# Optimization experiments

Measured on AMD Instinct MI355X. Metric: run time of the kernel, lower is better.

The kernel has to match this reference:

```python
import jax, jax.numpy as jnp
import numpy as np
from jax import lax

NPOINT, RADIUS, NSAMPLE = 1024, 0.2, 32
BN_EPS = 1e-5


def square_distance(src, dst):
    # src [B,N,C], dst [B,M,C] -> [B,N,M] squared euclidean distances
    d = -2.0 * jnp.einsum('bnc,bmc->bnm', src, dst)
    d = d + jnp.sum(src ** 2, -1)[:, :, None]
    d = d + jnp.sum(dst ** 2, -1)[:, None, :]
    return d


def index_points(points, idx):
    # points [B,N,C], idx [B,...] int -> [B,...,C]
    B = points.shape[0]
    bidx = jnp.arange(B).reshape((B,) + (1,) * (idx.ndim - 1))
    return points[bidx, idx]


def farthest_point_sample(xyz, npoint):
    # Deterministic variant: first centroid is point 0 (torch code uses randint).
    B, N, C = xyz.shape
    def step(carry, _):
        distance, farthest = carry
        centroid = jnp.take_along_axis(xyz, farthest[:, None, None], axis=1)  # [B,1,C]
        dist = jnp.sum((xyz - centroid) ** 2, -1)  # [B,N]
        distance = jnp.minimum(distance, dist)
        nxt = jnp.argmax(distance, -1).astype(jnp.int32)
        return (distance, nxt), farthest
    init = (jnp.full((B, N), 1e10, xyz.dtype), jnp.zeros((B,), jnp.int32))
    _, cents = lax.scan(step, init, None, length=npoint)  # [npoint, B]
    return cents.T  # [B, npoint]


def query_ball_point(radius, nsample, xyz, new_xyz):
    B, N, _ = xyz.shape
    sqr = square_distance(new_xyz, xyz)  # [B,M,N]
    gidx = jnp.where(sqr > radius ** 2, N, jnp.arange(N, dtype=jnp.int32))
    gidx = jnp.sort(gidx, axis=-1)[:, :, :nsample]  # [B,M,nsample]
    first = gidx[:, :, 0:1]
    return jnp.where(gidx == N, first, gidx)


def setup_inputs() -> dict:
    key = jax.random.key(0)
    ks = jax.random.split(key, 5)
    B, N, D = 16, 4096, 64
    xyz = jax.random.uniform(ks[0], (B, N, 3), dtype=jnp.float32)
    points = jax.random.normal(ks[1], (B, N, D), dtype=jnp.float32)
    W0 = jax.random.normal(ks[2], (64, 67), dtype=jnp.float32) * 0.05
    W1 = jax.random.normal(ks[3], (64, 64), dtype=jnp.float32) * 0.05
    W2 = jax.random.normal(ks[4], (128, 64), dtype=jnp.float32) * 0.05
    return {
        'xyz': xyz, 'points': points,
        'W0': W0, 'g0': jnp.ones((64,), jnp.float32), 'b0': jnp.zeros((64,), jnp.float32),
        'W1': W1, 'g1': jnp.ones((64,), jnp.float32), 'b1': jnp.zeros((64,), jnp.float32),
        'W2': W2, 'g2': jnp.ones((128,), jnp.float32), 'b2': jnp.zeros((128,), jnp.float32),
    }


def reference(xyz, points, W0, g0, b0, W1, g1, b1, W2, g2, b2):
    B, N, C = xyz.shape
    fps_idx = farthest_point_sample(xyz, NPOINT)             # [B,M]
    new_xyz = index_points(xyz, fps_idx)                     # [B,M,3]
    idx = query_ball_point(RADIUS, NSAMPLE, xyz, new_xyz)    # [B,M,S]
    grouped_xyz = index_points(xyz, idx) - new_xyz[:, :, None, :]   # [B,M,S,3]
    x = jnp.concatenate([index_points(points, idx), grouped_xyz], -1)  # [B,M,S,67]
    # shared 1x1 conv + BatchNorm (training-mode batch stats, biased var) + ReLU
    for W, g, b in ((W0, g0, b0), (W1, g1, b1), (W2, g2, b2)):
        x = jnp.einsum('bmsc,oc->bmso', x, W)
        mean = jnp.mean(x, axis=(0, 1, 2))
        var = jnp.var(x, axis=(0, 1, 2))
        x = jax.nn.relu((x - mean) * jax.lax.rsqrt(var + BN_EPS) * g + b)
    new_points = jnp.max(x, axis=2)  # max over nsample -> [B,M,128]
    return (new_xyz, new_points)
```

## Files before the change

kernel.cpp:

```cpp
#include <hip/hip_runtime.h>
#include <hip/hip_bf16.h>
#include <cstdint>
#include <cstddef>

namespace {
constexpr int B_ = 16;
constexpr int N_ = 4096;
constexpr int D_ = 64;
constexpr int M_ = 1024;
constexpr int S_ = 32;
constexpr int NROWS_ = B_ * M_ * S_;
constexpr int TPB_ = 256;
constexpr int NBLKM_ = NROWS_ / TPB_;
constexpr int NBLK2_ = NROWS_ / (2 * TPB_);
constexpr float RR_ = 0.04f;

constexpr size_t OFF_SQN  = 0;
constexpr size_t OFF_FPS  = 262144;
constexpr size_t OFF_BALL = 327680;
constexpr size_t OFF_W0T  = 2424832;
constexpr size_t OFF_W1T  = OFF_W0T + 67 * 64 * 4;
constexpr size_t OFF_W2T  = OFF_W1T + 64 * 64 * 4;
constexpr size_t OFF_PART = OFF_W2T + 64 * 128 * 4;
constexpr size_t OFF_BNP  = OFF_PART + (size_t)NBLKM_ * 256 * 4;
constexpr size_t OFF_E    = (OFF_BNP + 3072 + 255) & ~(size_t)255;
constexpr size_t E_SZ     = (size_t)B_ * N_ * 64 * 4;
constexpr size_t OFF_D    = OFF_E + E_SZ;
constexpr size_t D_SZ     = (size_t)B_ * M_ * 64 * 4;
constexpr size_t OFF_H1   = OFF_D + D_SZ;
constexpr size_t H1F_SZ   = (size_t)NROWS_ * 64 * 4;
constexpr size_t H1H_SZ   = (size_t)NROWS_ * 64 * 2;
constexpr size_t NEED_A   = OFF_H1 + H1F_SZ;
constexpr size_t NEED_B   = OFF_H1 + H1H_SZ;
}

__device__ __forceinline__ float mul_nr(float a, float b) {
    float p = a * b;
    asm("" : "+v"(p));
    return p;
}
__device__ __forceinline__ float mul_nf(float a, float b) {
    float p = a * b;
    asm volatile("" : "+v"(p));
    return p;
}

template <int CTRL>
__device__ __forceinline__ float dpp_movf(float x) {
    return __int_as_float(
        __builtin_amdgcn_update_dpp(0, __float_as_int(x), CTRL, 0xF, 0xF, true));
}
__device__ __forceinline__ float xor_exch(float x, int k) {
    if (k == 0) return dpp_movf<0xB1>(x);
    if (k == 1) return dpp_movf<0x4E>(x);
    return __shfl_xor(x, 1 << k);
}

__device__ __forceinline__ float fold_sum_wave(float* cur, int lane) {
#pragma unroll
    for (int k = 0; k < 6; k++) {
        const bool hi = (lane >> k) & 1;
#pragma unroll
        for (int m = 0; m < (32 >> k); m++) {
            const float a = cur[2 * m], b = cur[2 * m + 1];
            const float keep = hi ? b : a;
            const float give = hi ? a : b;
            const float got = xor_exch(give, k);
            cur[m] = keep + got;
        }
    }
    return cur[0];
}
__device__ __forceinline__ float fold_sum32(float* cur, int lane) {
#pragma unroll
    for (int k = 0; k < 5; k++) {
        const bool hi = (lane >> k) & 1;
#pragma unroll
        for (int m = 0; m < (16 >> k); m++) {
            const float a = cur[2 * m], b = cur[2 * m + 1];
            const float keep = hi ? b : a;
            const float give = hi ? a : b;
            const float got = xor_exch(give, k);
            cur[m] = keep + got;
        }
    }
    return cur[0];
}
__device__ __forceinline__ float fold_max32(float* cur, int lane) {
#pragma unroll
    for (int k = 0; k < 5; k++) {
        const bool hi = (lane >> k) & 1;
#pragma unroll
        for (int m = 0; m < (16 >> k); m++) {
            const float a = cur[2 * m], b = cur[2 * m + 1];
            const float keep = hi ? b : a;
            const float give = hi ? a : b;
            const float got = xor_exch(give, k);
            cur[m] = fmaxf(keep, got);
        }
    }
    return cur[0];
}
__device__ __forceinline__ float fold_min32(float* cur, int lane) {
#pragma unroll
    for (int k = 0; k < 5; k++) {
        const bool hi = (lane >> k) & 1;
#pragma unroll
        for (int m = 0; m < (16 >> k); m++) {
            const float a = cur[2 * m], b = cur[2 * m + 1];
            const float keep = hi ? b : a;
            const float give = hi ? a : b;
            const float got = xor_exch(give, k);
            cur[m] = fminf(keep, got);
        }
    }
    return cur[0];
}
__device__ __forceinline__ void fold_max_half(float* cur, int lane, float& r0, float& r1) {
#pragma unroll
    for (int k = 0; k < 5; k++) {
        const bool hi = (lane >> k) & 1;
#pragma unroll
        for (int m = 0; m < (32 >> k); m++) {
            const float a = cur[2 * m], b = cur[2 * m + 1];
            const float keep = hi ? b : a;
            const float give = hi ? a : b;
            const float got = xor_exch(give, k);
            cur[m] = fmaxf(keep, got);
        }
    }
    r0 = cur[0]; r1 = cur[1];
}

__device__ __forceinline__ unsigned short f2bf(float f) {
    __hip_bfloat16 h = __float2bfloat16(f);
    return *reinterpret_cast<unsigned short*>(&h);
}
__device__ __forceinline__ float bf2f(unsigned short u) {
    __hip_bfloat16 h = *reinterpret_cast<__hip_bfloat16*>(&u);
    return __bfloat162float(h);
}

__global__ __launch_bounds__(256) void k_sqnorm(const float* __restrict__ xyz,
                                                float* __restrict__ sqn) {
    int i = blockIdx.x * 256 + threadIdx.x;
    if (i >= B_ * N_) return;
    float x = xyz[3 * i], y = xyz[3 * i + 1], z = xyz[3 * i + 2];
    sqn[i] = (mul_nf(x, x) + mul_nf(y, y)) + mul_nf(z, z);
}

__global__ __launch_bounds__(512) void k_fps(const float* __restrict__ xyz,
                                             int* __restrict__ fps_idx) {
    const int b = blockIdx.x, t = threadIdx.x;
    const int lane = t & 63, w = t >> 6;
    const float* xb = xyz + (size_t)b * N_ * 3;
    __shared__ float pts[N_ * 3];
    __shared__ unsigned long long slots[2][8];
    for (int i = t; i < N_ * 3; i += 512) pts[i] = xb[i];
    __syncthreads();

    const int n0 = t * 8;
    float px[8], py[8], pz[8], dist[8];
#pragma unroll
    for (int k = 0; k < 8; k++) {
        px[k] = pts[3 * (n0 + k)];
        py[k] = pts[3 * (n0 + k) + 1];
        pz[k] = pts[3 * (n0 + k) + 2];
        dist[k] = 1e10f;
    }

    int far = 0;
    for (int i = 0; i < M_; i++) {
        if (t == 0) fps_idx[b * M_ + i] = far;
        const float c0 = pts[3 * far], c1 = pts[3 * far + 1], c2 = pts[3 * far + 2];
        float bestv = -1.0f; int bestn = n0;
#pragma unroll
        for (int k = 0; k < 8; k++) {
            const float d0 = px[k] - c0, d1 = py[k] - c1, d2 = pz[k] - c2;
            const float dd = (mul_nr(d0, d0) + mul_nr(d1, d1)) + mul_nr(d2, d2);
            const float dm = fminf(dist[k], dd);
            dist[k] = dm;
            if (dm > bestv) { bestv = dm; bestn = n0 + k; }
        }
        float m = bestv;
        m = fmaxf(m, dpp_movf<0x111>(m));
        m = fmaxf(m, dpp_movf<0x112>(m));
        m = fmaxf(m, dpp_movf<0x114>(m));
        m = fmaxf(m, dpp_movf<0x118>(m));
        m = fmaxf(m, dpp_movf<0x142>(m));
        m = fmaxf(m, dpp_movf<0x143>(m));
        const float wmax = __int_as_float(
            __builtin_amdgcn_readlane(__float_as_int(m), 63));
        const unsigned long long mk = __ballot(bestv == wmax);
        const int src = __ffsll((long long)mk) - 1;
        const int wn = __builtin_amdgcn_readlane(bestn, src);
        if (lane == 0)
            slots[i & 1][w] =
                ((unsigned long long)__float_as_uint(wmax) << 32) | (unsigned)(~wn);
        __syncthreads();
        const unsigned long long* sl = slots[i & 1];
        const unsigned long long s0 = sl[0], s1 = sl[1], s2 = sl[2], s3 = sl[3];
        const unsigned long long s4 = sl[4], s5 = sl[5], s6 = sl[6], s7 = sl[7];
        const unsigned long long a0 = s0 > s1 ? s0 : s1;
        const unsigned long long a1 = s2 > s3 ? s2 : s3;
        const unsigned long long a2 = s4 > s5 ? s4 : s5;
        const unsigned long long a3 = s6 > s7 ? s6 : s7;
        const unsigned long long b0 = a0 > a1 ? a0 : a1;
        const unsigned long long b1 = a2 > a3 ? a2 : a3;
        const unsigned long long bb = b0 > b1 ? b0 : b1;
        far = (int)(~(unsigned)bb);
    }
}

__global__ __launch_bounds__(256) void k_newxyz(const float* __restrict__ xyz,
                                                const int* __restrict__ fps_idx,
                                                float* __restrict__ newxyz) {
    int i = blockIdx.x * 256 + threadIdx.x;
    if (i >= B_ * M_) return;
    int b = i >> 10;
    int f = fps_idx[i];
    const float* p = xyz + ((size_t)b * N_ + f) * 3;
    newxyz[3 * i] = p[0]; newxyz[3 * i + 1] = p[1]; newxyz[3 * i + 2] = p[2];
}

__global__ __launch_bounds__(256) void k_ball(const float* __restrict__ xyz,
                                              const float* __restrict__ sqn,
                                              const int* __restrict__ fps_idx,
                                              const float* __restrict__ newxyz,
                                              int* __restrict__ ball) {
    const int w = threadIdx.x >> 6, lane = threadIdx.x & 63;
    const int q = blockIdx.x * 4 + w;
    const int b = q >> 10;
    __shared__ int buf[4][32];
    const float* xb = xyz + (size_t)b * N_ * 3;
    const float* sb = sqn + (size_t)b * N_;
    const float q0 = newxyz[3 * q], q1 = newxyz[3 * q + 1], q2 = newxyz[3 * q + 2];
    const float sq = sb[fps_idx[q]];

    int cnt = 0;
    for (int base = 0; base < N_ && cnt < 32; base += 64) {
        const int n = base + lane;
        const float p0 = xb[3 * n], p1 = xb[3 * n + 1], p2 = xb[3 * n + 2];
        float dot = fmaf(q2, p2, fmaf(q1, p1, q0 * p0));
        float tt = -2.0f * dot;
        tt = tt + sq;
        tt = tt + sb[n];
        const bool pred = !(tt > RR_);
        const unsigned long long mask = __ballot(pred);
        const int pos = cnt + __popcll(mask & ((1ull << lane) - 1ull));
        if (pred && pos < 32) buf[w][pos] = n;
        cnt += (int)__popcll(mask);
    }
    __syncthreads();
    if (lane < 32) {
        int e = buf[w][(lane < cnt) ? lane : 0];
        ball[(size_t)q * 32 + lane] = e;
    }
}

__global__ __launch_bounds__(256) void k_wtrans(const float* __restrict__ W0,
                                                const float* __restrict__ W1,
                                                const float* __restrict__ W2,
                                                float* __restrict__ W0T,
                                                float* __restrict__ W1T,
                                                float* __restrict__ W2T) {
    int t = blockIdx.x * 256 + threadIdx.x;
    if (t < 64 * 67) { int o = t / 67, c = t % 67; W0T[c * 64 + o] = W0[t]; }
    if (t < 64 * 64) { int o = t / 64, c = t % 64; W1T[c * 64 + o] = W1[t]; }
    if (t < 128 * 64) { int o = t / 64, c = t % 64; W2T[c * 128 + o] = W2[t]; }
}

__device__ __forceinline__ void stage_w(float* dst, const float* __restrict__ src,
                                        int n, int t) {
    for (int i = t; i < n; i += TPB_) dst[i] = src[i];
}

template <int NCH>
__device__ __forceinline__ void bn_relu(float* x, const float* __restrict__ bnp, int base) {
#pragma unroll
    for (int o = 0; o < NCH; o++)
        x[o] = fmaxf(0.f, fmaf(x[o], bnp[base + o], bnp[base + 128 + o]));
}

__device__ __forceinline__ void load_h0(float* x, const float* __restrict__ E,
                                        const float* __restrict__ Dq,
                                        const int* __restrict__ ball, int r) {
    const int b = r >> 15, q = r >> 5;
    const int g = ball[r];
    const float4* e = (const float4*)(E + ((size_t)(b * N_) + g) * 64);
    const float4* d = (const float4*)(Dq + (size_t)q * 64);
#pragma unroll
    for (int j = 0; j < 16; j++) {
        const float4 ev = e[j]; const float4 dv = d[j];
        x[4 * j + 0] = ev.x - dv.x; x[4 * j + 1] = ev.y - dv.y;
        x[4 * j + 2] = ev.z - dv.z; x[4 * j + 3] = ev.w - dv.w;
    }
}

__device__ __forceinline__ void h1_load_f32(float* x, const float* buf, int r) {
    const float4* src = (const float4*)(buf + (size_t)r * 64);
#pragma unroll
    for (int j = 0; j < 16; j++) {
        const float4 v = src[j];
        x[4 * j] = v.x; x[4 * j + 1] = v.y; x[4 * j + 2] = v.z; x[4 * j + 3] = v.w;
    }
}
__device__ __forceinline__ void h1_load_bf(float* x, const unsigned short* buf, int r) {
    const ushort4* src = (const ushort4*)(buf + (size_t)r * 64);
#pragma unroll
    for (int j = 0; j < 16; j++) {
        const ushort4 v = src[j];
        x[4 * j] = bf2f(v.x); x[4 * j + 1] = bf2f(v.y);
        x[4 * j + 2] = bf2f(v.z); x[4 * j + 3] = bf2f(v.w);
    }
}

__global__ __launch_bounds__(TPB_) void k_e(
    const float* __restrict__ points, const float* __restrict__ xyz,
    const float* __restrict__ W0T, float* __restrict__ E) {
    __shared__ float w0[67 * 64];
    const int t = threadIdx.x;
    stage_w(w0, W0T, 67 * 64, t);
    __syncthreads();
    const int n = blockIdx.x * TPB_ + t;
    const float* prow = points + (size_t)n * 64;
    float h[64];
#pragma unroll
    for (int o = 0; o < 64; o++) h[o] = 0.f;
#pragma unroll
    for (int c = 0; c < 64; c += 4) {
        const float4 xv = *reinterpret_cast<const float4*>(prow + c);
        const float xs[4] = {xv.x, xv.y, xv.z, xv.w};
#pragma unroll
        for (int j = 0; j < 4; j++) {
            const float xc = xs[j];
            const float* wr = w0 + (c + j) * 64;
#pragma unroll
            for (int o = 0; o < 64; o++) h[o] = fmaf(xc, wr[o], h[o]);
        }
    }
    const float x0 = xyz[(size_t)n * 3], x1 = xyz[(size_t)n * 3 + 1], x2 = xyz[(size_t)n * 3 + 2];
#pragma unroll
    for (int o = 0; o < 64; o++) h[o] = fmaf(x0, w0[64 * 64 + o], h[o]);
#pragma unroll
    for (int o = 0; o < 64; o++) h[o] = fmaf(x1, w0[65 * 64 + o], h[o]);
#pragma unroll
    for (int o = 0; o < 64; o++) h[o] = fmaf(x2, w0[66 * 64 + o], h[o]);
    float4* dst = (float4*)(E + (size_t)n * 64);
#pragma unroll
    for (int j = 0; j < 16; j++)
        dst[j] = make_float4(h[4 * j], h[4 * j + 1], h[4 * j + 2], h[4 * j + 3]);
}

__global__ __launch_bounds__(256) void k_d(
    const float* __restrict__ newxyz, const float* __restrict__ W0T,
    float* __restrict__ Dq) {
    const int q = blockIdx.x * 256 + threadIdx.x;
    const float n0 = newxyz[3 * q], n1 = newxyz[3 * q + 1], n2 = newxyz[3 * q + 2];
    const float* wa = W0T + 64 * 64;
    const float* wb = W0T + 65 * 64;
    const float* wc = W0T + 66 * 64;
    float* dst = Dq + (size_t)q * 64;
#pragma unroll
    for (int o = 0; o < 64; o++)
        dst[o] = fmaf(n2, wc[o], fmaf(n1, wb[o], n0 * wa[o]));
}

__global__ __launch_bounds__(TPB_, 2) void k_s0(
    const float* __restrict__ E, const float* __restrict__ Dq,
    const int* __restrict__ ball, float* __restrict__ partials) {
    const int t = threadIdx.x, lane = t & 63, w = t >> 6;
    const int r0 = blockIdx.x * 512 + t, r1 = r0 + 256;
    __shared__ float ssum[4][64], ssq[4][64];
    float x0[64], x1[64];
    load_h0(x0, E, Dq, ball, r0);
    load_h0(x1, E, Dq, ball, r1);
#pragma unroll
    for (int i = 0; i < 64; i++) {
        const float sv_ = x0[i] + x1[i];
        x1[i] = x0[i] * x0[i] + x1[i] * x1[i];
        x0[i] = sv_;
    }
    const float sv = fold_sum_wave(x0, lane);
    const float qv = fold_sum_wave(x1, lane);
    ssum[w][lane] = sv; ssq[w][lane] = qv;
    __syncthreads();
    if (t < 64) {
        float* dst = partials + (size_t)blockIdx.x * 256;
        dst[t] = ssum[0][t] + ssum[1][t] + ssum[2][t] + ssum[3][t];
        dst[128 + t] = ssq[0][t] + ssq[1][t] + ssq[2][t] + ssq[3][t];
    }
}

template <int HST>
__global__ __launch_bounds__(TPB_, 2) void k_s1(
    const float* __restrict__ E, const float* __restrict__ Dq,
    const int* __restrict__ ball, const float* __restrict__ W1T,
    const float* __restrict__ bnp, float* __restrict__ partials,
    float* __restrict__ h1f, unsigned short* __restrict__ h1h) {
    __shared__ float w1[64 * 64];
    __shared__ float ssum[4][64], ssq[4][64];
    const int t = threadIdx.x, lane = t & 63, w = t >> 6;
    stage_w(w1, W1T, 64 * 64, t);
    const int r0 = blockIdx.x * 512 + t, r1 = r0 + 256;
    float x0[64], x1[64];
    load_h0(x0, E, Dq, ball, r0);
    bn_relu<64>(x0, bnp, 0);
    load_h0(x1, E, Dq, ball, r1);
    bn_relu<64>(x1, bnp, 0);
    __syncthreads();

#pragma unroll
    for (int tile = 0; tile < 2; tile++) {
        float a0[32], a1[32];
#pragma unroll
        for (int o = 0; o < 32; o++) { a0[o] = 0.f; a1[o] = 0.f; }
#pragma unroll
        for (int c = 0; c < 64; c++) {
            const float* wr = w1 + c * 64 + tile * 32;
            const float xc0 = x0[c], xc1 = x1[c];
#pragma unroll
            for (int o = 0; o < 32; o++) {
                a0[o] = fmaf(xc0, wr[o], a0[o]);
                a1[o] = fmaf(xc1, wr[o], a1[o]);
            }
        }
        if constexpr (HST == 1) {
            float4* d0 = (float4*)(h1f + (size_t)r0 * 64 + tile * 32);
            float4* d1 = (float4*)(h1f + (size_t)r1 * 64 + tile * 32);
#pragma unroll
            for (int j = 0; j < 8; j++) {
                d0[j] = make_float4(a0[4 * j], a0[4 * j + 1], a0[4 * j + 2], a0[4 * j + 3]);
                d1[j] = make_float4(a1[4 * j], a1[4 * j + 1], a1[4 * j + 2], a1[4 * j + 3]);
            }
        } else {
            ushort4* d0 = (ushort4*)(h1h + (size_t)r0 * 64 + tile * 32);
            ushort4* d1 = (ushort4*)(h1h + (size_t)r1 * 64 + tile * 32);
#pragma unroll
            for (int j = 0; j < 8; j++) {
                ushort4 v0, v1;
                v0.x = f2bf(a0[4 * j]); v0.y = f2bf(a0[4 * j + 1]);
                v0.z = f2bf(a0[4 * j + 2]); v0.w = f2bf(a0[4 * j + 3]);
                v1.x = f2bf(a1[4 * j]); v1.y = f2bf(a1[4 * j + 1]);
                v1.z = f2bf(a1[4 * j + 2]); v1.w = f2bf(a1[4 * j + 3]);
                d0[j] = v0; d1[j] = v1;
            }
        }
#pragma unroll
        for (int o = 0; o < 32; o++) {
            const float sv_ = a0[o] + a1[o];
            a1[o] = a0[o] * a0[o] + a1[o] * a1[o];
            a0[o] = sv_;
        }
        float sv = fold_sum32(a0, lane); sv += __shfl_xor(sv, 32);
        float qv = fold_sum32(a1, lane); qv += __shfl_xor(qv, 32);
        if (lane < 32) { ssum[w][tile * 32 + lane] = sv; ssq[w][tile * 32 + lane] = qv; }
    }
    __syncthreads();
    if (t < 64) {
        float* dst = partials + (size_t)blockIdx.x * 256;
        dst[t] = ssum[0][t] + ssum[1][t] + ssum[2][t] + ssum[3][t];
        dst[128 + t] = ssq[0][t] + ssq[1][t] + ssq[2][t] + ssq[3][t];
    }
}

template <int HLD>
__global__ __launch_bounds__(TPB_, 2) void k_s2(
    const float* __restrict__ h1f, const unsigned short* __restrict__ h1h,
    const float* __restrict__ W2T, const float* __restrict__ bnp,
    float* __restrict__ partials, float* __restrict__ maxb,
    float* __restrict__ minb) {
    __shared__ float w2[64 * 128];
    __shared__ float ssum[4][128], ssq[4][128];
    const int t = threadIdx.x, lane = t & 63, w = t >> 6;
    stage_w(w2, W2T, 64 * 128, t);
    const int r0 = blockIdx.x * 512 + t, r1 = r0 + 256;
    float x0[64], x1[64];
    if constexpr (HLD == 1) { h1_load_f32(x0, h1f, r0); h1_load_f32(x1, h1f, r1); }
    else { h1_load_bf(x0, h1h, r0); h1_load_bf(x1, h1h, r1); }
    bn_relu<64>(x0, bnp, 256);
    bn_relu<64>(x1, bnp, 256);
    __syncthreads();

    const int q0 = blockIdx.x * 16 + w * 2 + (lane >> 5);
#pragma unroll
    for (int tile = 0; tile < 4; tile++) {
        float a0[32], a1[32];
#pragma unroll
        for (int o = 0; o < 32; o++) { a0[o] = 0.f; a1[o] = 0.f; }
#pragma unroll
        for (int c = 0; c < 64; c++) {
            const float* wr = w2 + c * 128 + tile * 32;
            const float xc0 = x0[c], xc1 = x1[c];
#pragma unroll
            for (int o = 0; o < 32; o++) {
                a0[o] = fmaf(xc0, wr[o], a0[o]);
                a1[o] = fmaf(xc1, wr[o], a1[o]);
            }
        }
        {
            float c0[32];
#pragma unroll
            for (int o = 0; o < 32; o++) c0[o] = a0[o];
            const float mx = fold_max32(c0, lane);
#pragma unroll
            for (int o = 0; o < 32; o++) c0[o] = a0[o];
            const float mn = fold_min32(c0, lane);
            maxb[(size_t)q0 * 128 + tile * 32 + (lane & 31)] = mx;
            minb[(size_t)q0 * 128 + tile * 32 + (lane & 31)] = mn;
#pragma unroll
            for (int o = 0; o < 32; o++) c0[o] = a1[o];
            const float mx1 = fold_max32(c0, lane);
#pragma unroll
            for (int o = 0; o < 32; o++) c0[o] = a1[o];
            const float mn1 = fold_min32(c0, lane);
            maxb[(size_t)(q0 + 8) * 128 + tile * 32 + (lane & 31)] = mx1;
            minb[(size_t)(q0 + 8) * 128 + tile * 32 + (lane & 31)] = mn1;
        }
#pragma unroll
        for (int o = 0; o < 32; o++) {
            const float sv_ = a0[o] + a1[o];
            a1[o] = a0[o] * a0[o] + a1[o] * a1[o];
            a0[o] = sv_;
        }
        float sv = fold_sum32(a0, lane); sv += __shfl_xor(sv, 32);
        float qv = fold_sum32(a1, lane); qv += __shfl_xor(qv, 32);
        if (lane < 32) { ssum[w][tile * 32 + lane] = sv; ssq[w][tile * 32 + lane] = qv; }
    }
    __syncthreads();
    if (t < 128) {
        float* dst = partials + (size_t)blockIdx.x * 256;
        dst[t] = ssum[0][t] + ssum[1][t] + ssum[2][t] + ssum[3][t];
        dst[128 + t] = ssq[0][t] + ssq[1][t] + ssq[2][t] + ssq[3][t];
    }
}

__global__ __launch_bounds__(256) void k_s3m(
    const float* __restrict__ maxb, const float* __restrict__ minb,
    const float* __restrict__ bnp, float* __restrict__ out_np) {
    const int i = blockIdx.x * 256 + threadIdx.x;
    const int ch = i & 127;
    const float sc = bnp[512 + ch], sh = bnp[512 + 128 + ch];
    const float h = (sc >= 0.f) ? maxb[i] : minb[i];
    out_np[i] = fmaxf(0.f, fmaf(h, sc, sh));
}

__device__ __forceinline__ void g0_row(
    const float* __restrict__ points, const float* __restrict__ xyz,
    const float* __restrict__ newxyz, const int* __restrict__ ball,
    const float* w0, int r, float* h0) {
    const int b = r >> 15;
    const int q = r >> 5;
    const int g = ball[r];
    const float* prow = points + ((size_t)(b * N_) + g) * D_;
    const float xg0 = xyz[((size_t)b * N_ + g) * 3 + 0] - newxyz[(size_t)q * 3 + 0];
    const float xg1 = xyz[((size_t)b * N_ + g) * 3 + 1] - newxyz[(size_t)q * 3 + 1];
    const float xg2 = xyz[((size_t)b * N_ + g) * 3 + 2] - newxyz[(size_t)q * 3 + 2];
#pragma unroll
    for (int o = 0; o < 64; o++) h0[o] = 0.f;
#pragma unroll
    for (int c = 0; c < 64; c += 4) {
        const float4 xv = *reinterpret_cast<const float4*>(prow + c);
        const float xs[4] = {xv.x, xv.y, xv.z, xv.w};
#pragma unroll
        for (int j = 0; j < 4; j++) {
            const float xc = xs[j];
            const float* wr = w0 + (c + j) * 64;
#pragma unroll
            for (int o = 0; o < 64; o++) h0[o] = fmaf(xc, wr[o], h0[o]);
        }
    }
#pragma unroll
    for (int o = 0; o < 64; o++) h0[o] = fmaf(xg0, w0[64 * 64 + o], h0[o]);
#pragma unroll
    for (int o = 0; o < 64; o++) h0[o] = fmaf(xg1, w0[65 * 64 + o], h0[o]);
#pragma unroll
    for (int o = 0; o < 64; o++) h0[o] = fmaf(xg2, w0[66 * 64 + o], h0[o]);
}

__device__ __forceinline__ void g1_row(const float* x, const float* w1, float* h1) {
#pragma unroll
    for (int o = 0; o < 64; o++) h1[o] = 0.f;
#pragma unroll
    for (int c = 0; c < 64; c++) {
        const float xc = x[c];
        const float* wr = w1 + c * 64;
#pragma unroll
        for (int o = 0; o < 64; o++) h1[o] = fmaf(xc, wr[o], h1[o]);
    }
}
__device__ __forceinline__ void g2_row(const float* x, const float* w2, float* h2) {
#pragma unroll
    for (int o = 0; o < 128; o++) h2[o] = 0.f;
#pragma unroll
    for (int c = 0; c < 64; c++) {
        const float xc = x[c];
        const float* wr = w2 + c * 128;
#pragma unroll
        for (int o = 0; o < 128; o++) h2[o] = fmaf(xc, wr[o], h2[o]);
    }
}

__device__ __forceinline__ void stats64_fold(float* h, int lane, int w, int t,
                                             float (*ssum)[64], float (*ssq)[64],
                                             float* dst) {
    float tmp[64];
#pragma unroll
    for (int i = 0; i < 64; i++) tmp[i] = h[i] * h[i];
    const float s = fold_sum_wave(h, lane);
    const float q = fold_sum_wave(tmp, lane);
    ssum[w][lane] = s; ssq[w][lane] = q;
    __syncthreads();
    if (t < 64) {
        dst[t] = ssum[0][t] + ssum[1][t] + ssum[2][t] + ssum[3][t];
        dst[128 + t] = ssq[0][t] + ssq[1][t] + ssq[2][t] + ssq[3][t];
    }
}
__device__ __forceinline__ void stats128_fold(float* h2, int lane, int w, int t,
                                              float (*ssum)[128], float (*ssq)[128],
                                              float* dst) {
    float tmp[64];
#pragma unroll
    for (int i = 0; i < 64; i++) tmp[i] = h2[i] * h2[i];
    const float sA = fold_sum_wave(h2, lane);
    const float qA = fold_sum_wave(tmp, lane);
    ssum[w][lane] = sA; ssq[w][lane] = qA;
#pragma unroll
    for (int i = 0; i < 64; i++) tmp[i] = h2[64 + i] * h2[64 + i];
    const float sB = fold_sum_wave(h2 + 64, lane);
    const float qB = fold_sum_wave(tmp, lane);
    ssum[w][64 + lane] = sB; ssq[w][64 + lane] = qB;
    __syncthreads();
    if (t < 128) {
        dst[t] = ssum[0][t] + ssum[1][t] + ssum[2][t] + ssum[3][t];
        dst[128 + t] = ssq[0][t] + ssq[1][t] + ssq[2][t] + ssq[3][t];
    }
}
__device__ __forceinline__ void max_out_r1(float* h2, int lane, int w, int blk,
                                           float* __restrict__ out_np) {
    const int qq = blk * 8 + w * 2 + (lane >> 5);
    float r0, r1;
    fold_max_half(h2, lane, r0, r1);
    out_np[(size_t)qq * 128 + (lane & 31)] = r0;
    out_np[(size_t)qq * 128 + 32 + (lane & 31)] = r1;
    fold_max_half(h2 + 64, lane, r0, r1);
    out_np[(size_t)qq * 128 + 64 + (lane & 31)] = r0;
    out_np[(size_t)qq * 128 + 96 + (lane & 31)] = r1;
}

__global__ __launch_bounds__(TPB_) void k_s0r(
    const float* __restrict__ points, const float* __restrict__ xyz,
    const float* __restrict__ newxyz, const int* __restrict__ ball,
    const float* __restrict__ W0T, float* __restrict__ partials) {
    __shared__ float w0[67 * 64];
    __shared__ float ssum[4][64], ssq[4][64];
    const int t = threadIdx.x, lane = t & 63, w = t >> 6;
    stage_w(w0, W0T, 67 * 64, t);
    __syncthreads();
    const int r = blockIdx.x * TPB_ + t;
    float h0[64];
    g0_row(points, xyz, newxyz, ball, w0, r, h0);
    stats64_fold(h0, lane, w, t, ssum, ssq, partials + (size_t)blockIdx.x * 256);
}
__global__ __launch_bounds__(TPB_) void k_s1r(
    const float* __restrict__ points, const float* __restrict__ xyz,
    const float* __restrict__ newxyz, const int* __restrict__ ball,
    const float* __restrict__ W0T, const float* __restrict__ W1T,
    const float* __restrict__ bnp, float* __restrict__ partials) {
    __shared__ float w0[67 * 64];
    __shared__ float w1[64 * 64];
    __shared__ float ssum[4][64], ssq[4][64];
    const int t = threadIdx.x, lane = t & 63, w = t >> 6;
    stage_w(w0, W0T, 67 * 64, t);
    stage_w(w1, W1T, 64 * 64, t);
    __syncthreads();
    const int r = blockIdx.x * TPB_ + t;
    float h0[64];
    g0_row(points, xyz, newxyz, ball, w0, r, h0);
    bn_relu<64>(h0, bnp, 0);
    float h1[64];
    g1_row(h0, w1, h1);
    stats64_fold(h1, lane, w, t, ssum, ssq, partials + (size_t)blockIdx.x * 256);
}
__global__ __launch_bounds__(TPB_) void k_s2r(
    const float* __restrict__ points, const float* __restrict__ xyz,
    const float* __restrict__ newxyz, const int* __restrict__ ball,
    const float* __restrict__ W0T, const float* __restrict__ W1T,
    const float* __restrict__ W2T, const float* __restrict__ bnp,
    float* __restrict__ partials) {
    __shared__ float w0[67 * 64];
    __shared__ float w1[64 * 64];
    __shared__ float w2[64 * 128];
    __shared__ float ssum[4][128], ssq[4][128];
    const int t = threadIdx.x, lane = t & 63, w = t >> 6;
    stage_w(w0, W0T, 67 * 64, t);
    stage_w(w1, W1T, 64 * 64, t);
    stage_w(w2, W2T, 64 * 128, t);
    __syncthreads();
    const int r = blockIdx.x * TPB_ + t;
    float h0[64];
    g0_row(points, xyz, newxyz, ball, w0, r, h0);
    bn_relu<64>(h0, bnp, 0);
    float h1[64];
    g1_row(h0, w1, h1);
    bn_relu<64>(h1, bnp, 256);
    float h2[128];
    g2_row(h1, w2, h2);
    stats128_fold(h2, lane, w, t, ssum, ssq, partials + (size_t)blockIdx.x * 256);
}
__global__ __launch_bounds__(TPB_) void k_s3r(
    const float* __restrict__ points, const float* __restrict__ xyz,
    const float* __restrict__ newxyz, const int* __restrict__ ball,
    const float* __restrict__ W0T, const float* __restrict__ W1T,
    const float* __restrict__ W2T, const float* __restrict__ bnp,
    float* __restrict__ out_np) {
    __shared__ float w0[67 * 64];
    __shared__ float w1[64 * 64];
    __shared__ float w2[64 * 128];
    const int t = threadIdx.x, lane = t & 63, w = t >> 6;
    stage_w(w0, W0T, 67 * 64, t);
    stage_w(w1, W1T, 64 * 64, t);
    stage_w(w2, W2T, 64 * 128, t);
    __syncthreads();
    const int r = blockIdx.x * TPB_ + t;
    float h0[64];
    g0_row(points, xyz, newxyz, ball, w0, r, h0);
    bn_relu<64>(h0, bnp, 0);
    float h1[64];
    g1_row(h0, w1, h1);
    bn_relu<64>(h1, bnp, 256);
    float h2[128];
    g2_row(h1, w2, h2);
    bn_relu<128>(h2, bnp, 512);
    max_out_r1(h2, lane, w, blockIdx.x, out_np);
}

template <int C, int NB>
__global__ __launch_bounds__(128) void k_bnfin(const float* __restrict__ partials,
                                               const float* __restrict__ gw,
                                               const float* __restrict__ bw,
                                               float* __restrict__ bnpL) {
    const int t = threadIdx.x;
    if (t >= C) return;
    double Ssum = 0.0, Q = 0.0;
    for (int blk = 0; blk < NB; blk++) {
        Ssum += (double)partials[(size_t)blk * 256 + t];
        Q += (double)partials[(size_t)blk * 256 + 128 + t];
    }
    const double mean = Ssum / (double)NROWS_;
    const double var = Q / (double)NROWS_ - mean * mean;
    const float sc = (float)((double)gw[t] / sqrt(var + 1e-5));
    const float sh = (float)((double)bw[t] - mean * (double)sc);
    bnpL[t] = sc;
    bnpL[128 + t] = sh;
}

extern "C" void kernel_launch(void* const* d_in, const int* in_sizes, int n_in,
                              void* d_out, int out_size, void* d_ws, size_t ws_size,
                              hipStream_t stream) {
    const float* xyz = (const float*)d_in[0];
    const float* points = (const float*)d_in[1];
    const float* W0 = (const float*)d_in[2];
    const float* g0 = (const float*)d_in[3];
    const float* b0 = (const float*)d_in[4];
    const float* W1 = (const float*)d_in[5];
    const float* g1 = (const float*)d_in[6];
    const float* b1 = (const float*)d_in[7];
    const float* W2 = (const float*)d_in[8];
    const float* g2 = (const float*)d_in[9];
    const float* b2 = (const float*)d_in[10];

    float* out = (float*)d_out;
    float* newxyz = out;
    float* out_np = out + B_ * M_ * 3;

    char* ws = (char*)d_ws;
    float* sqn = (float*)(ws + OFF_SQN);
    int* fps_idx = (int*)(ws + OFF_FPS);
    int* ball = (int*)(ws + OFF_BALL);
    float* W0T = (float*)(ws + OFF_W0T);
    float* W1T = (float*)(ws + OFF_W1T);
    float* W2T = (float*)(ws + OFF_W2T);
    float* partials = (float*)(ws + OFF_PART);
    float* bnp = (float*)(ws + OFF_BNP);
    float* Ebuf = (float*)(ws + OFF_E);
    float* Dbuf = (float*)(ws + OFF_D);
    float* h1f = (float*)(ws + OFF_H1);
    unsigned short* h1h = (unsigned short*)(ws + OFF_H1);
    float* maxb = (float*)(ws + OFF_E);
    float* minb = maxb + (size_t)B_ * M_ * 128;

    k_sqnorm<<<(B_ * N_ + 255) / 256, 256, 0, stream>>>(xyz, sqn);
    k_fps<<<B_, 512, 0, stream>>>(xyz, fps_idx);
    k_newxyz<<<(B_ * M_ + 255) / 256, 256, 0, stream>>>(xyz, fps_idx, newxyz);
    k_ball<<<B_ * M_ / 4, 256, 0, stream>>>(xyz, sqn, fps_idx, newxyz, ball);
    k_wtrans<<<32, 256, 0, stream>>>(W0, W1, W2, W0T, W1T, W2T);

    if (ws_size >= NEED_B) {
        k_e<<<B_ * N_ / TPB_, TPB_, 0, stream>>>(points, xyz, W0T, Ebuf);
        k_d<<<B_ * M_ / 256, 256, 0, stream>>>(newxyz, W0T, Dbuf);
        k_s0<<<NBLK2_, TPB_, 0, stream>>>(Ebuf, Dbuf, ball, partials);
        k_bnfin<64, NBLK2_><<<1, 128, 0, stream>>>(partials, g0, b0, bnp);
        if (ws_size >= NEED_A) {
            k_s1<1><<<NBLK2_, TPB_, 0, stream>>>(Ebuf, Dbuf, ball, W1T, bnp, partials, h1f, h1h);
            k_bnfin<64, NBLK2_><<<1, 128, 0, stream>>>(partials, g1, b1, bnp + 256);
            k_s2<1><<<NBLK2_, TPB_, 0, stream>>>(h1f, h1h, W2T, bnp, partials, maxb, minb);
            k_bnfin<128, NBLK2_><<<1, 128, 0, stream>>>(partials, g2, b2, bnp + 512);
            k_s3m<<<B_ * M_ * 128 / 256, 256, 0, stream>>>(maxb, minb, bnp, out_np);
        } else {
            k_s1<2><<<NBLK2_, TPB_, 0, stream>>>(Ebuf, Dbuf, ball, W1T, bnp, partials, h1f, h1h);
            k_bnfin<64, NBLK2_><<<1, 128, 0, stream>>>(partials, g1, b1, bnp + 256);
            k_s2<2><<<NBLK2_, TPB_, 0, stream>>>(h1f, h1h, W2T, bnp, partials, maxb, minb);
            k_bnfin<128, NBLK2_><<<1, 128, 0, stream>>>(partials, g2, b2, bnp + 512);
            k_s3m<<<B_ * M_ * 128 / 256, 256, 0, stream>>>(maxb, minb, bnp, out_np);
        }
    } else {
        k_s0r<<<NBLKM_, TPB_, 0, stream>>>(points, xyz, newxyz, ball, W0T, partials);
        k_bnfin<64, NBLKM_><<<1, 128, 0, stream>>>(partials, g0, b0, bnp);
        k_s1r<<<NBLKM_, TPB_, 0, stream>>>(points, xyz, newxyz, ball, W0T, W1T, bnp, partials);
        k_bnfin<64, NBLKM_><<<1, 128, 0, stream>>>(partials, g1, b1, bnp + 256);
        k_s2r<<<NBLKM_, TPB_, 0, stream>>>(points, xyz, newxyz, ball, W0T, W1T, W2T, bnp, partials);
        k_bnfin<128, NBLKM_><<<1, 128, 0, stream>>>(partials, g2, b2, bnp + 512);
        k_s3r<<<NBLKM_, TPB_, 0, stream>>>(points, xyz, newxyz, ball, W0T, W1T, W2T, bnp, out_np);
    }
}
```

Before: 1.254 ms.

## Overlap FPS with embedding precompute in one prelude kernel and parallelize BN finalize

Merges FPS, the per-point W0 embedding, squared norms and weight transposes into a single heterogeneous prelude launch, so the serial 16-block FPS runs alongside the other independent work instead of leaving most of the GPU idle. The FPS loop now carries the winning centroid's coordinates through the cross-wave reduction, which removes a dependent shared-memory load of the centroid each iteration. The newxyz gather and the D projection are fused into one kernel, and BN finalize switches from one block doing a serial double-precision sum to one block per channel with a tree reduction. The prelude's large shared-memory use for FPS applies to every block and may limit occupancy for the embedding blocks.

```diff
diff --git a/kernel.cpp b/kernel.cpp
--- a/kernel.cpp
+++ b/kernel.cpp
@@ -14,6 +14,12 @@
 constexpr int NBLKM_ = NROWS_ / TPB_;
 constexpr int NBLK2_ = NROWS_ / (2 * TPB_);
 constexpr float RR_ = 0.04f;
+
+constexpr int PRE_FPS = 16;
+constexpr int PRE_E   = 128;
+constexpr int PRE_SQ  = 128;
+constexpr int PRE_WT  = 1;
+constexpr int PRE_NB  = PRE_FPS + PRE_E + PRE_SQ + PRE_WT;
 
 constexpr size_t OFF_SQN  = 0;
 constexpr size_t OFF_FPS  = 262144;
@@ -141,21 +147,13 @@
     return __bfloat162float(h);
 }
 
-__global__ __launch_bounds__(256) void k_sqnorm(const float* __restrict__ xyz,
-                                                float* __restrict__ sqn) {
-    int i = blockIdx.x * 256 + threadIdx.x;
-    if (i >= B_ * N_) return;
-    float x = xyz[3 * i], y = xyz[3 * i + 1], z = xyz[3 * i + 2];
-    sqn[i] = (mul_nf(x, x) + mul_nf(y, y)) + mul_nf(z, z);
-}
-
-__global__ __launch_bounds__(512) void k_fps(const float* __restrict__ xyz,
-                                             int* __restrict__ fps_idx) {
-    const int b = blockIdx.x, t = threadIdx.x;
+__device__ void fps_body(const float* __restrict__ xyz, int* __restrict__ fps_idx, int b) {
+    const int t = threadIdx.x;
     const int lane = t & 63, w = t >> 6;
     const float* xb = xyz + (size_t)b * N_ * 3;
     __shared__ float pts[N_ * 3];
-    __shared__ unsigned long long slots[2][8];
+    __shared__ float4 slotA[2][8];
+    __shared__ float  slotZ[2][8];
     for (int i = t; i < N_ * 3; i += 512) pts[i] = xb[i];
     __syncthreads();
 
@@ -168,19 +166,28 @@
         pz[k] = pts[3 * (n0 + k) + 2];
         dist[k] = 1e10f;
     }
-
+    float c0 = pts[0], c1 = pts[1], c2 = pts[2];
     int far = 0;
+
     for (int i = 0; i < M_; i++) {
         if (t == 0) fps_idx[b * M_ + i] = far;
-        const float c0 = pts[3 * far], c1 = pts[3 * far + 1], c2 = pts[3 * far + 2];
-        float bestv = -1.0f; int bestn = n0;
+        float bestv = -1.0f;
 #pragma unroll
         for (int k = 0; k < 8; k++) {
             const float d0 = px[k] - c0, d1 = py[k] - c1, d2 = pz[k] - c2;
             const float dd = (mul_nr(d0, d0) + mul_nr(d1, d1)) + mul_nr(d2, d2);
             const float dm = fminf(dist[k], dd);
             dist[k] = dm;
-            if (dm > bestv) { bestv = dm; bestn = n0 + k; }
+            bestv = fmaxf(bestv, dm);
+        }
+        int kb = 7;
+#pragma unroll
+        for (int k = 6; k >= 0; k--) kb = (dist[k] == bestv) ? k : kb;
+        float sx = px[7], sy = py[7], sz = pz[7];
+#pragma unroll
+        for (int k = 6; k >= 0; k--) {
+            const bool e = (kb == k);
+            sx = e ? px[k] : sx; sy = e ? py[k] : sy; sz = e ? pz[k] : sz;
         }
         float m = bestv;
         m = fmaxf(m, dpp_movf<0x111>(m));
@@ -193,34 +200,130 @@
             __builtin_amdgcn_readlane(__float_as_int(m), 63));
         const unsigned long long mk = __ballot(bestv == wmax);
         const int src = __ffsll((long long)mk) - 1;
-        const int wn = __builtin_amdgcn_readlane(bestn, src);
-        if (lane == 0)
-            slots[i & 1][w] =
-                ((unsigned long long)__float_as_uint(wmax) << 32) | (unsigned)(~wn);
+        if (lane == src) {
+            float4 s;
+            s.x = __uint_as_float(~(unsigned)(n0 + kb));
+            s.y = wmax;
+            s.z = sx; s.w = sy;
+            slotA[i & 1][w] = s;
+            slotZ[i & 1][w] = sz;
+        }
         __syncthreads();
-        const unsigned long long* sl = slots[i & 1];
-        const unsigned long long s0 = sl[0], s1 = sl[1], s2 = sl[2], s3 = sl[3];
-        const unsigned long long s4 = sl[4], s5 = sl[5], s6 = sl[6], s7 = sl[7];
-        const unsigned long long a0 = s0 > s1 ? s0 : s1;
-        const unsigned long long a1 = s2 > s3 ? s2 : s3;
-        const unsigned long long a2 = s4 > s5 ? s4 : s5;
-        const unsigned long long a3 = s6 > s7 ? s6 : s7;
-        const unsigned long long b0 = a0 > a1 ? a0 : a1;
-        const unsigned long long b1 = a2 > a3 ? a2 : a3;
-        const unsigned long long bb = b0 > b1 ? b0 : b1;
-        far = (int)(~(unsigned)bb);
-    }
-}
-
-__global__ __launch_bounds__(256) void k_newxyz(const float* __restrict__ xyz,
-                                                const int* __restrict__ fps_idx,
-                                                float* __restrict__ newxyz) {
-    int i = blockIdx.x * 256 + threadIdx.x;
-    if (i >= B_ * M_) return;
-    int b = i >> 10;
-    int f = fps_idx[i];
+        const float4* sa = slotA[i & 1];
+        const float* szp = slotZ[i & 1];
+        unsigned long long K[8];
+        float CX[8], CY[8], CZ[8];
+#pragma unroll
+        for (int j = 0; j < 8; j++) {
+            const float4 s = sa[j];
+            K[j] = ((unsigned long long)__float_as_uint(s.y) << 32) |
+                   (unsigned long long)__float_as_uint(s.x);
+            CX[j] = s.z; CY[j] = s.w; CZ[j] = szp[j];
+        }
+#pragma unroll
+        for (int st = 1; st < 8; st <<= 1) {
+#pragma unroll
+            for (int j = 0; j < 8; j += 2 * st) {
+                const bool g = K[j + st] > K[j];
+                K[j]  = g ? K[j + st]  : K[j];
+                CX[j] = g ? CX[j + st] : CX[j];
+                CY[j] = g ? CY[j + st] : CY[j];
+                CZ[j] = g ? CZ[j + st] : CZ[j];
+            }
+        }
+        far = (int)(~(unsigned)K[0]);
+        c0 = CX[0]; c1 = CY[0]; c2 = CZ[0];
+    }
+}
+
+__device__ void e_body(const float* __restrict__ points, const float* __restrict__ xyz,
+                       const float* __restrict__ W0, float* __restrict__ E, int eb) {
+    __shared__ float w0[67 * 64];
+    const int t = threadIdx.x;
+    for (int i = t; i < 67 * 64; i += 512) {
+        const int c = i >> 6, o = i & 63;
+        w0[i] = W0[o * 67 + c];
+    }
+    __syncthreads();
+    const int n = eb * 512 + t;
+    const float* prow = points + (size_t)n * 64;
+    float h[64];
+#pragma unroll
+    for (int o = 0; o < 64; o++) h[o] = 0.f;
+#pragma unroll
+    for (int c = 0; c < 64; c += 4) {
+        const float4 xv = *reinterpret_cast<const float4*>(prow + c);
+        const float xs[4] = {xv.x, xv.y, xv.z, xv.w};
+#pragma unroll
+        for (int j = 0; j < 4; j++) {
+            const float xc = xs[j];
+            const float* wr = w0 + (c + j) * 64;
+#pragma unroll
+            for (int o = 0; o < 64; o++) h[o] = fmaf(xc, wr[o], h[o]);
+        }
+    }
+    const float x0 = xyz[(size_t)n * 3], x1 = xyz[(size_t)n * 3 + 1], x2 = xyz[(size_t)n * 3 + 2];
+#pragma unroll
+    for (int o = 0; o < 64; o++) h[o] = fmaf(x0, w0[64 * 64 + o], h[o]);
+#pragma unroll
+    for (int o = 0; o < 64; o++) h[o] = fmaf(x1, w0[65 * 64 + o], h[o]);
+#pragma unroll
+    for (int o = 0; o < 64; o++) h[o] = fmaf(x2, w0[66 * 64 + o], h[o]);
+    float4* dst = (float4*)(E + (size_t)n * 64);
+#pragma unroll
+    for (int j = 0; j < 16; j++)
+        dst[j] = make_float4(h[4 * j], h[4 * j + 1], h[4 * j + 2], h[4 * j + 3]);
+}
+
+__device__ void sq_body(const float* __restrict__ xyz, float* __restrict__ sqn, int sb) {
+    const int i = sb * 512 + threadIdx.x;
+    const float x = xyz[3 * i], y = xyz[3 * i + 1], z = xyz[3 * i + 2];
+    sqn[i] = (mul_nf(x, x) + mul_nf(y, y)) + mul_nf(z, z);
+}
+
+__device__ void wt_body(const float* __restrict__ W0, const float* __restrict__ W1,
+                        const float* __restrict__ W2, float* __restrict__ W0T,
+                        float* __restrict__ W1T, float* __restrict__ W2T) {
+    const int t = threadIdx.x;
+    for (int i = t; i < 67 * 64; i += 512) { const int c = i >> 6, o = i & 63; W0T[i] = W0[o * 67 + c]; }
+    for (int i = t; i < 64 * 64; i += 512) { const int c = i >> 6, o = i & 63; W1T[i] = W1[o * 64 + c]; }
+    for (int i = t; i < 64 * 128; i += 512) { const int c = i >> 7, o = i & 127; W2T[i] = W2[o * 64 + c]; }
+}
+
+__global__ __launch_bounds__(512) void k_prelude(
+    const float* __restrict__ xyz, const float* __restrict__ points,
+    const float* __restrict__ W0, const float* __restrict__ W1,
+    const float* __restrict__ W2, int* __restrict__ fps_idx,
+    float* __restrict__ E, float* __restrict__ sqn,
+    float* __restrict__ W0T, float* __restrict__ W1T, float* __restrict__ W2T,
+    int do_e) {
+    const int blk = blockIdx.x;
+    if (blk < PRE_FPS) { fps_body(xyz, fps_idx, blk); return; }
+    if (blk < PRE_FPS + PRE_E) { if (do_e) e_body(points, xyz, W0, E, blk - PRE_FPS); return; }
+    if (blk < PRE_FPS + PRE_E + PRE_SQ) { sq_body(xyz, sqn, blk - PRE_FPS - PRE_E); return; }
+    wt_body(W0, W1, W2, W0T, W1T, W2T);
+}
+
+__global__ __launch_bounds__(256) void k_nd(const float* __restrict__ xyz,
+                                            const int* __restrict__ fps_idx,
+                                            const float* __restrict__ W0T,
+                                            float* __restrict__ newxyz,
+                                            float* __restrict__ Dq, int do_d) {
+    const int w = threadIdx.x >> 6, lane = threadIdx.x & 63;
+    const int q = blockIdx.x * 4 + w;
+    const int b = q >> 10;
+    const int f = fps_idx[q];
     const float* p = xyz + ((size_t)b * N_ + f) * 3;
-    newxyz[3 * i] = p[0]; newxyz[3 * i + 1] = p[1]; newxyz[3 * i + 2] = p[2];
+    const float n0 = p[0], n1 = p[1], n2 = p[2];
+    if (lane == 0) {
+        newxyz[3 * q] = n0; newxyz[3 * q + 1] = n1; newxyz[3 * q + 2] = n2;
+    }
+    if (do_d) {
+        const float wa = W0T[64 * 64 + lane];
+        const float wb = W0T[65 * 64 + lane];
+        const float wc = W0T[66 * 64 + lane];
+        Dq[(size_t)q * 64 + lane] = fmaf(n2, wc, fmaf(n1, wb, n0 * wa));
+    }
 }
 
 __global__ __launch_bounds__(256) void k_ball(const float* __restrict__ xyz,
@@ -258,18 +361,6 @@
     }
 }
 
-__global__ __launch_bounds__(256) void k_wtrans(const float* __restrict__ W0,
-                                                const float* __restrict__ W1,
-                                                const float* __restrict__ W2,
-                                                float* __restrict__ W0T,
-                                                float* __restrict__ W1T,
-                                                float* __restrict__ W2T) {
-    int t = blockIdx.x * 256 + threadIdx.x;
-    if (t < 64 * 67) { int o = t / 67, c = t % 67; W0T[c * 64 + o] = W0[t]; }
-    if (t < 64 * 64) { int o = t / 64, c = t % 64; W1T[c * 64 + o] = W1[t]; }
-    if (t < 128 * 64) { int o = t / 64, c = t % 64; W2T[c * 128 + o] = W2[t]; }
-}
-
 __device__ __forceinline__ void stage_w(float* dst, const float* __restrict__ src,
                                         int n, int t) {
     for (int i = t; i < n; i += TPB_) dst[i] = src[i];
@@ -313,57 +404,6 @@
         x[4 * j] = bf2f(v.x); x[4 * j + 1] = bf2f(v.y);
         x[4 * j + 2] = bf2f(v.z); x[4 * j + 3] = bf2f(v.w);
     }
-}
-
-__global__ __launch_bounds__(TPB_) void k_e(
-    const float* __restrict__ points, const float* __restrict__ xyz,
-    const float* __restrict__ W0T, float* __restrict__ E) {
-    __shared__ float w0[67 * 64];
-    const int t = threadIdx.x;
-    stage_w(w0, W0T, 67 * 64, t);
-    __syncthreads();
-    const int n = blockIdx.x * TPB_ + t;
-    const float* prow = points + (size_t)n * 64;
-    float h[64];
-#pragma unroll
-    for (int o = 0; o < 64; o++) h[o] = 0.f;
-#pragma unroll
-    for (int c = 0; c < 64; c += 4) {
-        const float4 xv = *reinterpret_cast<const float4*>(prow + c);
-        const float xs[4] = {xv.x, xv.y, xv.z, xv.w};
-#pragma unroll
-        for (int j = 0; j < 4; j++) {
-            const float xc = xs[j];
-            const float* wr = w0 + (c + j) * 64;
-#pragma unroll
-            for (int o = 0; o < 64; o++) h[o] = fmaf(xc, wr[o], h[o]);
-        }
-    }
-    const float x0 = xyz[(size_t)n * 3], x1 = xyz[(size_t)n * 3 + 1], x2 = xyz[(size_t)n * 3 + 2];
-#pragma unroll
-    for (int o = 0; o < 64; o++) h[o] = fmaf(x0, w0[64 * 64 + o], h[o]);
-#pragma unroll
-    for (int o = 0; o < 64; o++) h[o] = fmaf(x1, w0[65 * 64 + o], h[o]);
-#pragma unroll
-    for (int o = 0; o < 64; o++) h[o] = fmaf(x2, w0[66 * 64 + o], h[o]);
-    float4* dst = (float4*)(E + (size_t)n * 64);
-#pragma unroll
-    for (int j = 0; j < 16; j++)
-        dst[j] = make_float4(h[4 * j], h[4 * j + 1], h[4 * j + 2], h[4 * j + 3]);
-}
-
-__global__ __launch_bounds__(256) void k_d(
-    const float* __restrict__ newxyz, const float* __restrict__ W0T,
-    float* __restrict__ Dq) {
-    const int q = blockIdx.x * 256 + threadIdx.x;
-    const float n0 = newxyz[3 * q], n1 = newxyz[3 * q + 1], n2 = newxyz[3 * q + 2];
-    const float* wa = W0T + 64 * 64;
-    const float* wb = W0T + 65 * 64;
-    const float* wc = W0T + 66 * 64;
-    float* dst = Dq + (size_t)q * 64;
-#pragma unroll
-    for (int o = 0; o < 64; o++)
-        dst[o] = fmaf(n2, wc[o], fmaf(n1, wb[o], n0 * wa[o]));
 }
 
 __global__ __launch_bounds__(TPB_, 2) void k_s0(
@@ -577,7 +617,6 @@
 #pragma unroll
     for (int o = 0; o < 64; o++) h0[o] = fmaf(xg2, w0[66 * 64 + o], h0[o]);
 }
-
 __device__ __forceinline__ void g1_row(const float* x, const float* w1, float* h1) {
 #pragma unroll
     for (int o = 0; o < 64; o++) h1[o] = 0.f;
@@ -600,7 +639,6 @@
         for (int o = 0; o < 128; o++) h2[o] = fmaf(xc, wr[o], h2[o]);
     }
 }
-
 __device__ __forceinline__ void stats64_fold(float* h, int lane, int w, int t,
                                              float (*ssum)[64], float (*ssq)[64],
                                              float* dst) {
@@ -647,7 +685,6 @@
     out_np[(size_t)qq * 128 + 64 + (lane & 31)] = r0;
     out_np[(size_t)qq * 128 + 96 + (lane & 31)] = r1;
 }
-
 __global__ __launch_bounds__(TPB_) void k_s0r(
     const float* __restrict__ points, const float* __restrict__ xyz,
     const float* __restrict__ newxyz, const int* __restrict__ ball,
@@ -736,23 +773,32 @@
 }
 
 template <int C, int NB>
-__global__ __launch_bounds__(128) void k_bnfin(const float* __restrict__ partials,
+__global__ __launch_bounds__(256) void k_bnfin(const float* __restrict__ partials,
                                                const float* __restrict__ gw,
                                                const float* __restrict__ bw,
                                                float* __restrict__ bnpL) {
+    const int ch = blockIdx.x;
     const int t = threadIdx.x;
-    if (t >= C) return;
-    double Ssum = 0.0, Q = 0.0;
-    for (int blk = 0; blk < NB; blk++) {
-        Ssum += (double)partials[(size_t)blk * 256 + t];
-        Q += (double)partials[(size_t)blk * 256 + 128 + t];
-    }
-    const double mean = Ssum / (double)NROWS_;
-    const double var = Q / (double)NROWS_ - mean * mean;
-    const float sc = (float)((double)gw[t] / sqrt(var + 1e-5));
-    const float sh = (float)((double)bw[t] - mean * (double)sc);
-    bnpL[t] = sc;
-    bnpL[128 + t] = sh;
+    double s = 0.0, q = 0.0;
+    for (int blk = t; blk < NB; blk += 256) {
+        s += (double)partials[(size_t)blk * 256 + ch];
+        q += (double)partials[(size_t)blk * 256 + 128 + ch];
+    }
+    __shared__ double ls[256], lq[256];
+    ls[t] = s; lq[t] = q;
+    __syncthreads();
+    for (int off = 128; off >= 1; off >>= 1) {
+        if (t < off) { ls[t] += ls[t + off]; lq[t] += lq[t + off]; }
+        __syncthreads();
+    }
+    if (t == 0) {
+        const double mean = ls[0] / (double)NROWS_;
+        const double var = lq[0] / (double)NROWS_ - mean * mean;
+        const float sc = (float)((double)gw[ch] / sqrt(var + 1e-5));
+        const float sh = (float)((double)bw[ch] - mean * (double)sc);
+        bnpL[ch] = sc;
+        bnpL[128 + ch] = sh;
+    }
 }
 
 extern "C" void kernel_launch(void* const* d_in, const int* in_sizes, int n_in,
@@ -790,37 +836,34 @@
     float* maxb = (float*)(ws + OFF_E);
     float* minb = maxb + (size_t)B_ * M_ * 128;
 
-    k_sqnorm<<<(B_ * N_ + 255) / 256, 256, 0, stream>>>(xyz, sqn);
-    k_fps<<<B_, 512, 0, stream>>>(xyz, fps_idx);
-    k_newxyz<<<(B_ * M_ + 255) / 256, 256, 0, stream>>>(xyz, fps_idx, newxyz);
+    const int cached = (ws_size >= NEED_B) ? 1 : 0;
+
+    k_prelude<<<PRE_NB, 512, 0, stream>>>(xyz, points, W0, W1, W2, fps_idx,
+                                          Ebuf, sqn, W0T, W1T, W2T, cached);
+    k_nd<<<B_ * M_ / 4, 256, 0, stream>>>(xyz, fps_idx, W0T, newxyz, Dbuf, cached);
     k_ball<<<B_ * M_ / 4, 256, 0, stream>>>(xyz, sqn, fps_idx, newxyz, ball);
-    k_wtrans<<<32, 256, 0, stream>>>(W0, W1, W2, W0T, W1T, W2T);
-
-    if (ws_size >= NEED_B) {
-        k_e<<<B_ * N_ / TPB_, TPB_, 0, stream>>>(points, xyz, W0T, Ebuf);
-        k_d<<<B_ * M_ / 256, 256, 0, stream>>>(newxyz, W0T, Dbuf);
+
+    if (cached) {
         k_s0<<<NBLK2_, TPB_, 0, stream>>>(Ebuf, Dbuf, ball, partials);
-        k_bnfin<64, NBLK2_><<<1, 128, 0, stream>>>(partials, g0, b0, bnp);
+        k_bnfin<64, NBLK2_><<<64, 256, 0, stream>>>(partials, g0, b0, bnp);
         if (ws_size >= NEED_A) {
             k_s1<1><<<NBLK2_, TPB_, 0, stream>>>(Ebuf, Dbuf, ball, W1T, bnp, partials, h1f, h1h);
-            k_bnfin<64, NBLK2_><<<1, 128, 0, stream>>>(partials, g1, b1, bnp + 256);
+            k_bnfin<64, NBLK2_><<<64, 256, 0, stream>>>(partials, g1, b1, bnp + 256);
             k_s2<1><<<NBLK2_, TPB_, 0, stream>>>(h1f, h1h, W2T, bnp, partials, maxb, minb);
-            k_bnfin<128, NBLK2_><<<1, 128, 0, stream>>>(partials, g2, b2, bnp + 512);
-            k_s3m<<<B_ * M_ * 128 / 256, 256, 0, stream>>>(maxb, minb, bnp, out_np);
         } else {
             k_s1<2><<<NBLK2_, TPB_, 0, stream>>>(Ebuf, Dbuf, ball, W1T, bnp, partials, h1f, h1h);
-            k_bnfin<64, NBLK2_><<<1, 128, 0, stream>>>(partials, g1, b1, bnp + 256);
+            k_bnfin<64, NBLK2_><<<64, 256, 0, stream>>>(partials, g1, b1, bnp + 256);
             k_s2<2><<<NBLK2_, TPB_, 0, stream>>>(h1f, h1h, W2T, bnp, partials, maxb, minb);
-            k_bnfin<128, NBLK2_><<<1, 128, 0, stream>>>(partials, g2, b2, bnp + 512);
-            k_s3m<<<B_ * M_ * 128 / 256, 256, 0, stream>>>(maxb, minb, bnp, out_np);
-        }
+        }
+        k_bnfin<128, NBLK2_><<<128, 256, 0, stream>>>(partials, g2, b2, bnp + 512);
+        k_s3m<<<B_ * M_ * 128 / 256, 256, 0, stream>>>(maxb, minb, bnp, out_np);
     } else {
         k_s0r<<<NBLKM_, TPB_, 0, stream>>>(points, xyz, newxyz, ball, W0T, partials);
-        k_bnfin<64, NBLKM_><<<1, 128, 0, stream>>>(partials, g0, b0, bnp);
+        k_bnfin<64, NBLKM_><<<64, 256, 0, stream>>>(partials, g0, b0, bnp);
         k_s1r<<<NBLKM_, TPB_, 0, stream>>>(points, xyz, newxyz, ball, W0T, W1T, bnp, partials);
-        k_bnfin<64, NBLKM_><<<1, 128, 0, stream>>>(partials, g1, b1, bnp + 256);
+        k_bnfin<64, NBLKM_><<<64, 256, 0, stream>>>(partials, g1, b1, bnp + 256);
         k_s2r<<<NBLKM_, TPB_, 0, stream>>>(points, xyz, newxyz, ball, W0T, W1T, W2T, bnp, partials);
-        k_bnfin<128, NBLKM_><<<1, 128, 0, stream>>>(partials, g2, b2, bnp + 512);
+        k_bnfin<128, NBLKM_><<<128, 256, 0, stream>>>(partials, g2, b2, bnp + 512);
         k_s3r<<<NBLKM_, TPB_, 0, stream>>>(points, xyz, newxyz, ball, W0T, W1T, W2T, bnp, out_np);
     }
 }
```

After: 1.413 ms. +12.7%, slower.
